# Kernel optimization log

Hardware: AMD Instinct MI355X
Metric: run time of the kernel (lower is better)

The kernel has to match this reference:

```python
import jax, jax.numpy as jnp
import numpy as np

MIN_DISTANCE = 1.0  # default forward arg of the torch module


def setup_inputs() -> dict:
    key = jax.random.key(0)
    k1, k2 = jax.random.split(key)
    B, N = 4, 4096
    coords = jax.random.normal(k1, (B, N, 3), dtype=jnp.float32) * 5.0
    steric_radii = jax.random.uniform(k2, (B, N), dtype=jnp.float32)
    return {"coords": coords, "steric_radii": steric_radii}


def reference(coords, steric_radii):
    # coords: [B,N,3], steric_radii: [B,N]
    diff = coords[:, :, None, :] - coords[:, None, :, :]          # [B,N,N,3]
    d2 = jnp.sum(diff * diff, axis=-1)                             # [B,N,N]
    # safe sqrt: exact 0 on the diagonal (matches torch.cdist), no NaN grads
    pairwise = jnp.where(d2 > 0, jnp.sqrt(jnp.where(d2 > 0, d2, 1.0)), 0.0)
    sr = steric_radii[:, :, None] + steric_radii[:, None, :]       # [B,N,N]
    target = jnp.maximum(MIN_DISTANCE, sr)
    penalty = jax.nn.relu(target - pairwise)[..., None]            # [B,N,N,1]
    direction = jnp.clip(diff, -1.0, 1.0)                          # [B,N,N,3]
    adjustment = jnp.mean(penalty * direction, axis=2)             # [B,N,3]
    return coords + 0.1 * adjustment
```

## Files before the change

kernel.cpp:

```cpp
#include <hip/hip_runtime.h>

#define BB 4
#define NN 4096
#define TI 256
#define JB 32
#define JLEN (NN / JB)

#if __has_builtin(__builtin_amdgcn_sqrtf)
  #define FAST_SQRT __builtin_amdgcn_sqrtf
#else
  #define FAST_SQRT sqrtf
#endif

__device__ __forceinline__ float clip1(float x) {
    return fminf(fmaxf(x, -1.0f), 1.0f);
}

#define PACK_ELEMS (BB * NN)
#define PART_OFF   (PACK_ELEMS * 4)

__global__ __launch_bounds__(256) void ncp_pack(
    const float* __restrict__ coords,
    const float* __restrict__ radii,
    float4* __restrict__ packed)
{
    const int t = blockIdx.x * 256 + threadIdx.x;
    if (t >= PACK_ELEMS) return;
    packed[t] = make_float4(coords[t * 3 + 0], coords[t * 3 + 1],
                            coords[t * 3 + 2], radii[t]);
}

__global__ __launch_bounds__(TI) void ncp_partial(
    const float4* __restrict__ packed,
    float* __restrict__ part)
{
    const int b = blockIdx.z;
    const int i = blockIdx.x * TI + threadIdx.x;
    const int s = blockIdx.y;
    const float4* jsrc = packed + b * NN + s * JLEN;

    const float4 me = packed[b * NN + i];
    const float xi = me.x, yi = me.y, zi = me.z, ri = me.w;

    float ax = 0.0f, ay = 0.0f, az = 0.0f;

    #pragma unroll 4
    for (int k = 0; k < JLEN; ++k) {
        const float4 c = jsrc[k];
        const float dx = xi - c.x;
        const float dy = yi - c.y;
        const float dz = zi - c.z;
        const float d2 = fmaf(dx, dx, fmaf(dy, dy, dz * dz));
        if (__any(d2 < 4.0f)) {
            const float dist = FAST_SQRT(d2);
            const float tgt = fmaxf(1.0f, ri + c.w);
            const float p = fmaxf(tgt - dist, 0.0f);
            ax = fmaf(p, clip1(dx), ax);
            ay = fmaf(p, clip1(dy), ay);
            az = fmaf(p, clip1(dz), az);
        }
    }

    float* dst = part + (size_t)s * (BB * NN * 3);
    const int o = (b * NN + i) * 3;
    dst[o + 0] = ax;
    dst[o + 1] = ay;
    dst[o + 2] = az;
}

__global__ __launch_bounds__(256) void ncp_reduce(
    const float* __restrict__ coords,
    const float* __restrict__ part,
    float* __restrict__ out)
{
    const int o = blockIdx.x * 256 + threadIdx.x;
    if (o >= BB * NN * 3) return;
    float acc = 0.0f;
    #pragma unroll
    for (int s = 0; s < JB; ++s)
        acc += part[(size_t)s * (BB * NN * 3) + o];
    out[o] = fmaf(0.1f / (float)NN, acc, coords[o]);
}

__global__ __launch_bounds__(TI) void ncp_direct(
    const float* __restrict__ coords,
    const float* __restrict__ radii,
    float* __restrict__ out)
{
    __shared__ float4 jt[TI];
    const int b = blockIdx.z;
    const int i = blockIdx.x * TI + threadIdx.x;

    const float xi = coords[(b * NN + i) * 3 + 0];
    const float yi = coords[(b * NN + i) * 3 + 1];
    const float zi = coords[(b * NN + i) * 3 + 2];
    const float ri = radii[b * NN + i];

    float ax = 0.0f, ay = 0.0f, az = 0.0f;

    for (int jc = 0; jc < NN; jc += TI) {
        const int jj = jc + threadIdx.x;
        __syncthreads();
        jt[threadIdx.x] = make_float4(coords[(b * NN + jj) * 3 + 0],
                                      coords[(b * NN + jj) * 3 + 1],
                                      coords[(b * NN + jj) * 3 + 2],
                                      radii[b * NN + jj]);
        __syncthreads();
        #pragma unroll 4
        for (int k = 0; k < TI; ++k) {
            const float4 c = jt[k];
            const float dx = xi - c.x;
            const float dy = yi - c.y;
            const float dz = zi - c.z;
            const float d2 = fmaf(dx, dx, fmaf(dy, dy, dz * dz));
            if (__any(d2 < 4.0f)) {
                const float dist = FAST_SQRT(d2);
                const float tgt = fmaxf(1.0f, ri + c.w);
                const float p = fmaxf(tgt - dist, 0.0f);
                ax = fmaf(p, clip1(dx), ax);
                ay = fmaf(p, clip1(dy), ay);
                az = fmaf(p, clip1(dz), az);
            }
        }
    }

    const int o = (b * NN + i) * 3;
    const float sc = 0.1f / (float)NN;
    out[o + 0] = fmaf(sc, ax, coords[o + 0]);
    out[o + 1] = fmaf(sc, ay, coords[o + 1]);
    out[o + 2] = fmaf(sc, az, coords[o + 2]);
}

extern "C" void kernel_launch(void* const* d_in, const int* in_sizes, int n_in,
                              void* d_out, int out_size, void* d_ws, size_t ws_size,
                              hipStream_t stream) {
    const float* coords = (const float*)d_in[0];
    const float* radii  = (const float*)d_in[1];
    float* out = (float*)d_out;
    const int n = BB * NN * 3;
    const size_t need = (size_t)(PART_OFF + (size_t)JB * n) * sizeof(float);

    if (ws_size >= need) {
        float4* packed = (float4*)d_ws;
        float* part = (float*)d_ws + PART_OFF;
        ncp_pack<<<(PACK_ELEMS + 255) / 256, 256, 0, stream>>>(coords, radii, packed);
        ncp_partial<<<dim3(NN / TI, JB, BB), TI, 0, stream>>>(packed, part);
        ncp_reduce<<<(n + 255) / 256, 256, 0, stream>>>(coords, part, out);
    } else {
        ncp_direct<<<dim3(NN / TI, 1, BB), TI, 0, stream>>>(coords, radii, out);
    }
}
```

Measured before the change: 81.12 us.

## Fuse partial and reduce kernels using in-block wave split of j range

Replaces the partial-sum kernel plus separate reduce kernel with one kernel. Each block of 16 waves handles 64 i-points, with each wave covering a slice of j, and the slices are reduced through shared memory. Squared distance is now computed via the norm expansion (|i|^2 + |j|^2 - 2 i·j) using precomputed norms, and j loads are software-prefetched in groups of four. This removes a launch and the global partial-buffer round trip, but it adds extra per-j loads and can lose precision in the expanded distance near the threshold.

```diff
diff --git a/kernel.cpp b/kernel.cpp
--- a/kernel.cpp
+++ b/kernel.cpp
@@ -2,9 +2,10 @@
 
 #define BB 4
 #define NN 4096
-#define TI 256
-#define JB 32
-#define JLEN (NN / JB)
+#define WPB 16
+#define TPB (WPB * 64)
+#define JPW (NN / WPB)
+#define GRP 4
 
 #if __has_builtin(__builtin_amdgcn_sqrtf)
   #define FAST_SQRT __builtin_amdgcn_sqrtf
@@ -17,79 +18,113 @@
 }
 
 #define PACK_ELEMS (BB * NN)
-#define PART_OFF   (PACK_ELEMS * 4)
+#define N2_OFF (PACK_ELEMS * 4)
 
 __global__ __launch_bounds__(256) void ncp_pack(
     const float* __restrict__ coords,
     const float* __restrict__ radii,
-    float4* __restrict__ packed)
+    float4* __restrict__ p4,
+    float* __restrict__ n2a)
 {
     const int t = blockIdx.x * 256 + threadIdx.x;
     if (t >= PACK_ELEMS) return;
-    packed[t] = make_float4(coords[t * 3 + 0], coords[t * 3 + 1],
-                            coords[t * 3 + 2], radii[t]);
+    const float x = coords[t * 3 + 0];
+    const float y = coords[t * 3 + 1];
+    const float z = coords[t * 3 + 2];
+    p4[t] = make_float4(x, y, z, radii[t]);
+    n2a[t] = fmaf(z, z, fmaf(y, y, x * x));
 }
 
-__global__ __launch_bounds__(TI) void ncp_partial(
-    const float4* __restrict__ packed,
-    float* __restrict__ part)
+__global__ __launch_bounds__(TPB, 4) void ncp_fused(
+    const float4* __restrict__ p4,
+    const float* __restrict__ n2a,
+    const float* __restrict__ coords,
+    float* __restrict__ out)
 {
+    __shared__ float sh[WPB][3][64];
+
     const int b = blockIdx.z;
-    const int i = blockIdx.x * TI + threadIdx.x;
-    const int s = blockIdx.y;
-    const float4* jsrc = packed + b * NN + s * JLEN;
+    const int ibase = blockIdx.x * 64;
+    const int lane = threadIdx.x & 63;
+    const int w = threadIdx.x >> 6;
+    const int i = ibase + lane;
 
-    const float4 me = packed[b * NN + i];
-    const float xi = me.x, yi = me.y, zi = me.z, ri = me.w;
+    const float4 me = p4[b * NN + i];
+    const float n2i = n2a[b * NN + i];
+    const float m2x = -2.0f * me.x;
+    const float m2y = -2.0f * me.y;
+    const float m2z = -2.0f * me.z;
+    const float ri = me.w;
+
+    const int jbase = __builtin_amdgcn_readfirstlane(w * JPW);
+    const float4* jp = p4  + b * NN + jbase;
+    const float*  jn = n2a + b * NN + jbase;
 
     float ax = 0.0f, ay = 0.0f, az = 0.0f;
 
-    #pragma unroll 4
-    for (int k = 0; k < JLEN; ++k) {
-        const float4 c = jsrc[k];
-        const float dx = xi - c.x;
-        const float dy = yi - c.y;
-        const float dz = zi - c.z;
-        const float d2 = fmaf(dx, dx, fmaf(dy, dy, dz * dz));
-        if (__any(d2 < 4.0f)) {
-            const float dist = FAST_SQRT(d2);
-            const float tgt = fmaxf(1.0f, ri + c.w);
-            const float p = fmaxf(tgt - dist, 0.0f);
-            ax = fmaf(p, clip1(dx), ax);
-            ay = fmaf(p, clip1(dy), ay);
-            az = fmaf(p, clip1(dz), az);
-        }
+    float4 c[GRP]; float nj[GRP];
+    #pragma unroll
+    for (int g = 0; g < GRP; ++g) { c[g] = jp[g]; nj[g] = jn[g]; }
+
+#define PROCESS(CC, NJ)                                                    \
+    _Pragma("unroll")                                                      \
+    for (int g = 0; g < GRP; ++g) {                                        \
+        const float sd = fmaf(m2z, CC[g].z,                                \
+                         fmaf(m2y, CC[g].y,                                \
+                         fmaf(m2x, CC[g].x, NJ[g])));                      \
+        const float d2v = sd + n2i;                                        \
+        if (__any(d2v < 4.0f)) {                                           \
+            const float dist = FAST_SQRT(fmaxf(d2v, 0.0f));                \
+            const float tgt  = fmaxf(1.0f, ri + CC[g].w);                  \
+            const float p    = fmaxf(tgt - dist, 0.0f);                    \
+            const float dx   = fmaf(-0.5f, m2x, -CC[g].x);                 \
+            const float dy   = fmaf(-0.5f, m2y, -CC[g].y);                 \
+            const float dz   = fmaf(-0.5f, m2z, -CC[g].z);                 \
+            ax = fmaf(p, clip1(dx), ax);                                   \
+            ay = fmaf(p, clip1(dy), ay);                                   \
+            az = fmaf(p, clip1(dz), az);                                   \
+        }                                                                  \
     }
 
-    float* dst = part + (size_t)s * (BB * NN * 3);
-    const int o = (b * NN + i) * 3;
-    dst[o + 0] = ax;
-    dst[o + 1] = ay;
-    dst[o + 2] = az;
+    for (int k0 = 0; k0 + GRP < JPW; k0 += GRP) {
+        float4 c2[GRP]; float nj2[GRP];
+        #pragma unroll
+        for (int g = 0; g < GRP; ++g) {
+            c2[g]  = jp[k0 + GRP + g];
+            nj2[g] = jn[k0 + GRP + g];
+        }
+        PROCESS(c, nj)
+        #pragma unroll
+        for (int g = 0; g < GRP; ++g) { c[g] = c2[g]; nj[g] = nj2[g]; }
+    }
+    PROCESS(c, nj)
+#undef PROCESS
+
+    sh[w][0][lane] = ax;
+    sh[w][1][lane] = ay;
+    sh[w][2][lane] = az;
+    __syncthreads();
+
+    if (threadIdx.x < 192) {
+        const int comp = threadIdx.x >> 6;
+        const int ii = threadIdx.x & 63;
+        float acc = 0.0f;
+        #pragma unroll
+        for (int ww = 0; ww < WPB; ++ww)
+            acc += sh[ww][comp][ii];
+        const int o = (b * NN + ibase + ii) * 3 + comp;
+        out[o] = fmaf(0.1f / (float)NN, acc, coords[o]);
+    }
 }
 
-__global__ __launch_bounds__(256) void ncp_reduce(
-    const float* __restrict__ coords,
-    const float* __restrict__ part,
-    float* __restrict__ out)
-{
-    const int o = blockIdx.x * 256 + threadIdx.x;
-    if (o >= BB * NN * 3) return;
-    float acc = 0.0f;
-    #pragma unroll
-    for (int s = 0; s < JB; ++s)
-        acc += part[(size_t)s * (BB * NN * 3) + o];
-    out[o] = fmaf(0.1f / (float)NN, acc, coords[o]);
-}
-
-__global__ __launch_bounds__(TI) void ncp_direct(
+__global__ __launch_bounds__(256) void ncp_direct(
     const float* __restrict__ coords,
     const float* __restrict__ radii,
     float* __restrict__ out)
 {
-    __shared__ float4 jt[TI];
+    __shared__ float4 jt[256];
     const int b = blockIdx.z;
-    const int i = blockIdx.x * TI + threadIdx.x;
+    const int i = blockIdx.x * 256 + threadIdx.x;
 
     const float xi = coords[(b * NN + i) * 3 + 0];
     const float yi = coords[(b * NN + i) * 3 + 1];
@@ -98,7 +133,7 @@
 
     float ax = 0.0f, ay = 0.0f, az = 0.0f;
 
-    for (int jc = 0; jc < NN; jc += TI) {
+    for (int jc = 0; jc < NN; jc += 256) {
         const int jj = jc + threadIdx.x;
         __syncthreads();
         jt[threadIdx.x] = make_float4(coords[(b * NN + jj) * 3 + 0],
@@ -107,15 +142,15 @@
                                       radii[b * NN + jj]);
         __syncthreads();
         #pragma unroll 4
-        for (int k = 0; k < TI; ++k) {
-            const float4 c = jt[k];
-            const float dx = xi - c.x;
-            const float dy = yi - c.y;
-            const float dz = zi - c.z;
+        for (int k = 0; k < 256; ++k) {
+            const float4 cc = jt[k];
+            const float dx = xi - cc.x;
+            const float dy = yi - cc.y;
+            const float dz = zi - cc.z;
             const float d2 = fmaf(dx, dx, fmaf(dy, dy, dz * dz));
             if (__any(d2 < 4.0f)) {
                 const float dist = FAST_SQRT(d2);
-                const float tgt = fmaxf(1.0f, ri + c.w);
+                const float tgt = fmaxf(1.0f, ri + cc.w);
                 const float p = fmaxf(tgt - dist, 0.0f);
                 ax = fmaf(p, clip1(dx), ax);
                 ay = fmaf(p, clip1(dy), ay);
@@ -137,16 +172,14 @@
     const float* coords = (const float*)d_in[0];
     const float* radii  = (const float*)d_in[1];
     float* out = (float*)d_out;
-    const int n = BB * NN * 3;
-    const size_t need = (size_t)(PART_OFF + (size_t)JB * n) * sizeof(float);
+    const size_t need = (size_t)(PACK_ELEMS * 5) * sizeof(float);
 
     if (ws_size >= need) {
-        float4* packed = (float4*)d_ws;
-        float* part = (float*)d_ws + PART_OFF;
-        ncp_pack<<<(PACK_ELEMS + 255) / 256, 256, 0, stream>>>(coords, radii, packed);
-        ncp_partial<<<dim3(NN / TI, JB, BB), TI, 0, stream>>>(packed, part);
-        ncp_reduce<<<(n + 255) / 256, 256, 0, stream>>>(coords, part, out);
+        float4* p4 = (float4*)d_ws;
+        float* n2a = (float*)d_ws + N2_OFF;
+        ncp_pack<<<(PACK_ELEMS + 255) / 256, 256, 0, stream>>>(coords, radii, p4, n2a);
+        ncp_fused<<<dim3(NN / 64, 1, BB), TPB, 0, stream>>>(p4, n2a, coords, out);
     } else {
-        ncp_direct<<<dim3(NN / TI, 1, BB), TI, 0, stream>>>(coords, radii, out);
+        ncp_direct<<<dim3(NN / 256, 1, BB), 256, 0, stream>>>(coords, radii, out);
     }
 }
```

New measurement: 83.80 us. 3.3% more time.
